# Kernel optimization log

Hardware: AMD Instinct MI355X
Metric: run time of the kernel (lower is better)

Reference implementation:

```python
import jax, jax.numpy as jnp
import numpy as np

GAMMA = 1.0  # offset scaling factor (init kwarg gamma)


def setup_inputs() -> dict:
    key = jax.random.key(0)
    k1, k2, k3 = jax.random.split(key, 3)
    B, C, L, n = 32, 256, 8192, 2048
    inp = jax.random.normal(k1, (B, C, L), dtype=jnp.float32)
    # sampling positions in pixel units, uniform over [0, L-1]
    point = jax.random.uniform(k2, (B, n, 1), dtype=jnp.float32) * (L - 1)
    offset = jax.random.normal(k3, (B, n, 1), dtype=jnp.float32)
    return {"input": inp, "point": point, "offset": offset}


def reference(input, point, offset):
    B, C, L = input.shape
    # (B, n) fractional sampling locations, clamped to valid range
    locs = jnp.clip(point[..., 0] + GAMMA * offset[..., 0], 0.0, L - 1)
    idx0 = jnp.clip(jnp.floor(locs).astype(jnp.int32), 0, L - 1)
    idx1 = jnp.clip(jnp.ceil(locs).astype(jnp.int32), 0, L - 1)
    w1 = locs - idx0.astype(locs.dtype)  # (B, n)
    w0 = 1.0 - w1
    # gather along length axis: (B, C, n)
    g0 = jnp.take_along_axis(input, idx0[:, None, :], axis=2)
    g1 = jnp.take_along_axis(input, idx1[:, None, :], axis=2)
    out = w0[:, None, :] * g0 + w1[:, None, :] * g1  # (B, C, n)
    return jnp.transpose(out, (0, 2, 1))  # (B, n, C)
```

## Files before the change

### kernel.cpp

```cpp
#include <hip/hip_runtime.h>


constexpr int   kB     = 32;
constexpr int   kC     = 256;
constexpr int   kL     = 8192;
constexpr int   kN     = 2048;
constexpr float kGamma = 1.0f;

constexpr int kLt   = 32;
constexpr int kT    = kL / kLt;
constexpr int kCap  = 64;
constexpr int kNXCD = 8;

__global__ __launch_bounds__(256) void fused_sampler_kernel(
    const float* __restrict__ input,
    const float* __restrict__ point,
    const float* __restrict__ offset,
    float* __restrict__ out)
{
    constexpr int kStride = kLt + 1;
    __shared__ float lds[kC * kStride];
    __shared__ int2  mlist[kCap];
    __shared__ int   mcnt;

    constexpr int nwg = kB * kT;
    constexpr int cpx = nwg / kNXCD;
    int wg = blockIdx.x;
    wg = (wg % kNXCD) * cpx + wg / kNXCD;

    const int b   = wg >> 8;
    const int t   = wg & (kT - 1);
    const int tid = threadIdx.x;

    if (tid == 0) mcnt = 0;
    __syncthreads();

    const float* base = input + (size_t)b * kC * kL + t * kLt;
    float4 vals[8];
    #pragma unroll
    for (int k = 0; k < 8; ++k) {
        const int flat4 = k * 256 + tid;
        const int c     = flat4 >> 3;
        const int col4  = flat4 & 7;
        vals[k] = *reinterpret_cast<const float4*>(base + (size_t)c * kL + col4 * 4);
    }
    int gcol = t * kLt + kLt;
    if (gcol > kL - 1) gcol = kL - 1;
    const float halo = input[((size_t)(b * kC + tid)) * kL + gcol];

    {
        const int p0 = tid * 8;
        const float* pp = point  + (size_t)b * kN + p0;
        const float* op = offset + (size_t)b * kN + p0;
        const float4 pA = *reinterpret_cast<const float4*>(pp);
        const float4 pB = *reinterpret_cast<const float4*>(pp + 4);
        const float4 oA = *reinterpret_cast<const float4*>(op);
        const float4 oB = *reinterpret_cast<const float4*>(op + 4);
        float locs[8] = { pA.x + kGamma * oA.x, pA.y + kGamma * oA.y,
                          pA.z + kGamma * oA.z, pA.w + kGamma * oA.w,
                          pB.x + kGamma * oB.x, pB.y + kGamma * oB.y,
                          pB.z + kGamma * oB.z, pB.w + kGamma * oB.w };
        #pragma unroll
        for (int j = 0; j < 8; ++j) {
            float loc = fminf(fmaxf(locs[j], 0.0f), (float)(kL - 1));
            const int idx0 = (int)floorf(loc);
            if ((idx0 >> 5) == t) {
                const int slot = atomicAdd(&mcnt, 1);
                if (slot < kCap)
                    mlist[slot] = make_int2(p0 + j, __float_as_int(loc));
            }
        }
    }

    #pragma unroll
    for (int k = 0; k < 8; ++k) {
        const int flat4 = k * 256 + tid;
        const int c     = flat4 >> 3;
        const int col4  = flat4 & 7;
        float* dst = &lds[c * kStride + col4 * 4];
        dst[0] = vals[k].x; dst[1] = vals[k].y; dst[2] = vals[k].z; dst[3] = vals[k].w;
    }
    lds[tid * kStride + kLt] = halo;
    __syncthreads();

    const int cnt = min(mcnt, kCap);
    for (int e = 0; e < cnt; ++e) {
        const int2 ent  = mlist[e];
        const int   p    = ent.x;
        const float loc  = __int_as_float(ent.y);
        const int   idx0 = (int)floorf(loc);
        const float w1   = loc - (float)idx0;
        const float w0   = 1.0f - w1;
        const int   li   = idx0 - t * kLt;
        const float g0 = lds[tid * kStride + li];
        const float g1 = lds[tid * kStride + li + 1];
        out[((size_t)b * kN + p) * kC + tid] = w0 * g0 + w1 * g1;
    }
}

extern "C" void kernel_launch(void* const* d_in, const int* in_sizes, int n_in,
                              void* d_out, int out_size, void* d_ws, size_t ws_size,
                              hipStream_t stream)
{
    const float* input  = (const float*)d_in[0];
    const float* point  = (const float*)d_in[1];
    const float* offset = (const float*)d_in[2];
    float* out = (float*)d_out;

    fused_sampler_kernel<<<kB * kT, 256, 0, stream>>>(input, point, offset, out);
}
```

Measured before the change: 68.91 us.

## Process eight L-tiles per workgroup with register double-buffered prefetch

Each workgroup now walks eight consecutive 32-column tiles instead of one. While one tile is being sampled out of LDS, the next tile is held in registers and the one after is already being loaded. Point/offset binning is done once per group into per-tile lists, which removes the 8x redundant scan of all 2048 points that one-tile-per-workgroup needed. The grid shrinks to 1024 workgroups and the XCD remapping is dropped. In exchange the kernel uses more registers (occupancy hint of 4), has less parallelism, and caps each tile's list at 48 entries, which risks dropping points when a tile is dense.

```diff
diff --git a/kernel.cpp b/kernel.cpp
--- a/kernel.cpp
+++ b/kernel.cpp
@@ -7,12 +7,12 @@
 constexpr int   kN     = 2048;
 constexpr float kGamma = 1.0f;
 
-constexpr int kLt   = 32;
-constexpr int kT    = kL / kLt;
-constexpr int kCap  = 64;
-constexpr int kNXCD = 8;
+constexpr int kLt     = 32;
+constexpr int kTG     = 8;
+constexpr int kGroups = kL / (kLt * kTG);
+constexpr int kCap    = 48;
 
-__global__ __launch_bounds__(256) void fused_sampler_kernel(
+__global__ __launch_bounds__(256, 4) void fused_sampler_kernel(
     const float* __restrict__ input,
     const float* __restrict__ point,
     const float* __restrict__ offset,
@@ -20,33 +20,38 @@
 {
     constexpr int kStride = kLt + 1;
     __shared__ float lds[kC * kStride];
-    __shared__ int2  mlist[kCap];
-    __shared__ int   mcnt;
+    __shared__ int2  mlist[kTG][kCap];
+    __shared__ int   mcnt[kTG];
 
-    constexpr int nwg = kB * kT;
-    constexpr int cpx = nwg / kNXCD;
-    int wg = blockIdx.x;
-    wg = (wg % kNXCD) * cpx + wg / kNXCD;
+    const int wg  = blockIdx.x;
+    const int b   = wg >> 5;
+    const int tg  = wg & (kGroups - 1);
+    const int tid = threadIdx.x;
+    const int col0 = tg * (kLt * kTG);
 
-    const int b   = wg >> 8;
-    const int t   = wg & (kT - 1);
-    const int tid = threadIdx.x;
-
-    if (tid == 0) mcnt = 0;
+    if (tid < kTG) mcnt[tid] = 0;
     __syncthreads();
 
-    const float* base = input + (size_t)b * kC * kL + t * kLt;
-    float4 vals[8];
+    const float* bbase = input + (size_t)b * kC * kL;
+
+    float4 A[8], B[8];
     #pragma unroll
     for (int k = 0; k < 8; ++k) {
         const int flat4 = k * 256 + tid;
         const int c     = flat4 >> 3;
         const int col4  = flat4 & 7;
-        vals[k] = *reinterpret_cast<const float4*>(base + (size_t)c * kL + col4 * 4);
+        A[k] = *reinterpret_cast<const float4*>(bbase + (size_t)c * kL + col0 + col4 * 4);
     }
-    int gcol = t * kLt + kLt;
+    #pragma unroll
+    for (int k = 0; k < 8; ++k) {
+        const int flat4 = k * 256 + tid;
+        const int c     = flat4 >> 3;
+        const int col4  = flat4 & 7;
+        B[k] = *reinterpret_cast<const float4*>(bbase + (size_t)c * kL + col0 + kLt + col4 * 4);
+    }
+    int gcol = col0 + kLt * kTG;
     if (gcol > kL - 1) gcol = kL - 1;
-    const float halo = input[((size_t)(b * kC + tid)) * kL + gcol];
+    const float h7 = bbase[(size_t)tid * kL + gcol];
 
     {
         const int p0 = tid * 8;
@@ -56,46 +61,81 @@
         const float4 pB = *reinterpret_cast<const float4*>(pp + 4);
         const float4 oA = *reinterpret_cast<const float4*>(op);
         const float4 oB = *reinterpret_cast<const float4*>(op + 4);
-        float locs[8] = { pA.x + kGamma * oA.x, pA.y + kGamma * oA.y,
-                          pA.z + kGamma * oA.z, pA.w + kGamma * oA.w,
-                          pB.x + kGamma * oB.x, pB.y + kGamma * oB.y,
-                          pB.z + kGamma * oB.z, pB.w + kGamma * oB.w };
+        const float locs[8] = { pA.x + kGamma * oA.x, pA.y + kGamma * oA.y,
+                                pA.z + kGamma * oA.z, pA.w + kGamma * oA.w,
+                                pB.x + kGamma * oB.x, pB.y + kGamma * oB.y,
+                                pB.z + kGamma * oB.z, pB.w + kGamma * oB.w };
         #pragma unroll
         for (int j = 0; j < 8; ++j) {
             float loc = fminf(fmaxf(locs[j], 0.0f), (float)(kL - 1));
             const int idx0 = (int)floorf(loc);
-            if ((idx0 >> 5) == t) {
-                const int slot = atomicAdd(&mcnt, 1);
+            const int rng  = (idx0 >> 5) - tg * kTG;
+            if ((unsigned)rng < (unsigned)kTG) {
+                const int slot = atomicAdd(&mcnt[rng], 1);
                 if (slot < kCap)
-                    mlist[slot] = make_int2(p0 + j, __float_as_int(loc));
+                    mlist[rng][slot] = make_int2(p0 + j, __float_as_int(loc));
             }
         }
     }
 
-    #pragma unroll
-    for (int k = 0; k < 8; ++k) {
-        const int flat4 = k * 256 + tid;
-        const int c     = flat4 >> 3;
-        const int col4  = flat4 & 7;
-        float* dst = &lds[c * kStride + col4 * 4];
-        dst[0] = vals[k].x; dst[1] = vals[k].y; dst[2] = vals[k].z; dst[3] = vals[k].w;
-    }
-    lds[tid * kStride + kLt] = halo;
-    __syncthreads();
+    auto tile_phase = [&](const int tt, float4 (&curr)[8], float4 (&next)[8]) {
+        if (tt > 0) __syncthreads();
 
-    const int cnt = min(mcnt, kCap);
-    for (int e = 0; e < cnt; ++e) {
-        const int2 ent  = mlist[e];
-        const int   p    = ent.x;
-        const float loc  = __int_as_float(ent.y);
-        const int   idx0 = (int)floorf(loc);
-        const float w1   = loc - (float)idx0;
-        const float w0   = 1.0f - w1;
-        const int   li   = idx0 - t * kLt;
-        const float g0 = lds[tid * kStride + li];
-        const float g1 = lds[tid * kStride + li + 1];
-        out[((size_t)b * kN + p) * kC + tid] = w0 * g0 + w1 * g1;
-    }
+        #pragma unroll
+        for (int k = 0; k < 8; ++k) {
+            const int flat4 = k * 256 + tid;
+            const int c     = flat4 >> 3;
+            const int col4  = flat4 & 7;
+            float* dst = &lds[c * kStride + col4 * 4];
+            dst[0] = curr[k].x; dst[1] = curr[k].y; dst[2] = curr[k].z; dst[3] = curr[k].w;
+        }
+        if (tt < kTG - 1) {
+            if ((tid & 7) == 0) {
+                #pragma unroll
+                for (int k = 0; k < 8; ++k) {
+                    const int c = (k * 256 + tid) >> 3;
+                    lds[c * kStride + kLt] = next[k].x;
+                }
+            }
+        } else {
+            lds[tid * kStride + kLt] = h7;
+        }
+        __syncthreads();
+
+        if (tt < kTG - 2) {
+            const int colb = col0 + (tt + 2) * kLt;
+            #pragma unroll
+            for (int k = 0; k < 8; ++k) {
+                const int flat4 = k * 256 + tid;
+                const int c     = flat4 >> 3;
+                const int col4  = flat4 & 7;
+                curr[k] = *reinterpret_cast<const float4*>(bbase + (size_t)c * kL + colb + col4 * 4);
+            }
+        }
+
+        const int cnt = min(mcnt[tt], kCap);
+        for (int e = 0; e < cnt; ++e) {
+            const int2 ent  = mlist[tt][e];
+            const int   p    = ent.x;
+            const float loc  = __int_as_float(ent.y);
+            const int   idx0 = (int)floorf(loc);
+            const float w1   = loc - (float)idx0;
+            const float w0   = 1.0f - w1;
+            const int   li   = idx0 - (col0 + tt * kLt);
+            const float g0 = lds[tid * kStride + li];
+            const float g1 = lds[tid * kStride + li + 1];
+            out[((size_t)b * kN + p) * kC + tid] = w0 * g0 + w1 * g1;
+        }
+    };
+
+    tile_phase(0, A, B);
+    tile_phase(1, B, A);
+    tile_phase(2, A, B);
+    tile_phase(3, B, A);
+    tile_phase(4, A, B);
+    tile_phase(5, B, A);
+    tile_phase(6, A, B);
+    tile_phase(7, B, A);
 }
 
 extern "C" void kernel_launch(void* const* d_in, const int* in_sizes, int n_in,
@@ -107,5 +147,5 @@
     const float* offset = (const float*)d_in[2];
     float* out = (float*)d_out;
 
-    fused_sampler_kernel<<<kB * kT, 256, 0, stream>>>(input, point, offset, out);
+    fused_sampler_kernel<<<kB * kGroups, 256, 0, stream>>>(input, point, offset, out);
 }
```

Measured after the change: 69.05 us. No clear change (+0.2%).

## Split tiles by channel group and widen length tiles, parallelize point loop

Applied to the files above, without the earlier changes.

Each workgroup now handles 32 channels over a 128-column length tile instead of all 256 channels over 32 columns. The matched-point loop is spread across eight 32-lane groups, so each group processes different points. This shrinks LDS use to raise occupancy and gives longer contiguous row reads. In exchange, every workgroup still scans all point/offset data, doubling that redundant traffic, and output stores become 128-byte segments.

```diff
diff --git a/kernel.cpp b/kernel.cpp
--- a/kernel.cpp
+++ b/kernel.cpp
@@ -7,46 +7,54 @@
 constexpr int   kN     = 2048;
 constexpr float kGamma = 1.0f;
 
-constexpr int kLt   = 32;
+constexpr int kCh   = 32;
+constexpr int kCG   = kC / kCh;
+constexpr int kLt   = 128;
 constexpr int kT    = kL / kLt;
-constexpr int kCap  = 64;
+constexpr int kCap  = 96;
 constexpr int kNXCD = 8;
 
-__global__ __launch_bounds__(256) void fused_sampler_kernel(
+__global__ __launch_bounds__(256, 8) void fused_sampler_kernel(
     const float* __restrict__ input,
     const float* __restrict__ point,
     const float* __restrict__ offset,
     float* __restrict__ out)
 {
     constexpr int kStride = kLt + 1;
-    __shared__ float lds[kC * kStride];
+    __shared__ float lds[kCh * kStride];
     __shared__ int2  mlist[kCap];
     __shared__ int   mcnt;
 
-    constexpr int nwg = kB * kT;
+    constexpr int nwg = kB * kCG * kT;
     constexpr int cpx = nwg / kNXCD;
     int wg = blockIdx.x;
     wg = (wg % kNXCD) * cpx + wg / kNXCD;
 
-    const int b   = wg >> 8;
-    const int t   = wg & (kT - 1);
-    const int tid = threadIdx.x;
+    const int b    = wg >> 9;
+    const int rem  = wg & 511;
+    const int cg   = rem >> 6;
+    const int t    = rem & (kT - 1);
+    const int tid  = threadIdx.x;
 
     if (tid == 0) mcnt = 0;
     __syncthreads();
 
-    const float* base = input + (size_t)b * kC * kL + t * kLt;
-    float4 vals[8];
+    const float* base = input + (size_t)(b * kC + cg * kCh) * kL + t * kLt;
+
+    float4 v[4];
     #pragma unroll
-    for (int k = 0; k < 8; ++k) {
+    for (int k = 0; k < 4; ++k) {
         const int flat4 = k * 256 + tid;
-        const int c     = flat4 >> 3;
-        const int col4  = flat4 & 7;
-        vals[k] = *reinterpret_cast<const float4*>(base + (size_t)c * kL + col4 * 4);
+        const int row   = flat4 >> 5;
+        const int col4  = flat4 & 31;
+        v[k] = *reinterpret_cast<const float4*>(base + (size_t)row * kL + col4 * 4);
     }
-    int gcol = t * kLt + kLt;
-    if (gcol > kL - 1) gcol = kL - 1;
-    const float halo = input[((size_t)(b * kC + tid)) * kL + gcol];
+    float halo = 0.0f;
+    if (tid < kCh) {
+        int gc = t * kLt + kLt;
+        if (gc > kL - 1) gc = kL - 1;
+        halo = input[(size_t)(b * kC + cg * kCh + tid) * kL + gc];
+    }
 
     {
         const int p0 = tid * 8;
@@ -56,15 +64,16 @@
         const float4 pB = *reinterpret_cast<const float4*>(pp + 4);
         const float4 oA = *reinterpret_cast<const float4*>(op);
         const float4 oB = *reinterpret_cast<const float4*>(op + 4);
-        float locs[8] = { pA.x + kGamma * oA.x, pA.y + kGamma * oA.y,
-                          pA.z + kGamma * oA.z, pA.w + kGamma * oA.w,
-                          pB.x + kGamma * oB.x, pB.y + kGamma * oB.y,
-                          pB.z + kGamma * oB.z, pB.w + kGamma * oB.w };
+        const float locs[8] = { pA.x + kGamma * oA.x, pA.y + kGamma * oA.y,
+                                pA.z + kGamma * oA.z, pA.w + kGamma * oA.w,
+                                pB.x + kGamma * oB.x, pB.y + kGamma * oB.y,
+                                pB.z + kGamma * oB.z, pB.w + kGamma * oB.w };
         #pragma unroll
         for (int j = 0; j < 8; ++j) {
             float loc = fminf(fmaxf(locs[j], 0.0f), (float)(kL - 1));
             const int idx0 = (int)floorf(loc);
-            if ((idx0 >> 5) == t) {
+            const int li   = idx0 - t * kLt;
+            if ((unsigned)li < (unsigned)kLt) {
                 const int slot = atomicAdd(&mcnt, 1);
                 if (slot < kCap)
                     mlist[slot] = make_int2(p0 + j, __float_as_int(loc));
@@ -73,18 +82,20 @@
     }
 
     #pragma unroll
-    for (int k = 0; k < 8; ++k) {
+    for (int k = 0; k < 4; ++k) {
         const int flat4 = k * 256 + tid;
-        const int c     = flat4 >> 3;
-        const int col4  = flat4 & 7;
-        float* dst = &lds[c * kStride + col4 * 4];
-        dst[0] = vals[k].x; dst[1] = vals[k].y; dst[2] = vals[k].z; dst[3] = vals[k].w;
+        const int row   = flat4 >> 5;
+        const int col4  = flat4 & 31;
+        float* dst = &lds[row * kStride + col4 * 4];
+        dst[0] = v[k].x; dst[1] = v[k].y; dst[2] = v[k].z; dst[3] = v[k].w;
     }
-    lds[tid * kStride + kLt] = halo;
+    if (tid < kCh) lds[tid * kStride + kLt] = halo;
     __syncthreads();
 
     const int cnt = min(mcnt, kCap);
-    for (int e = 0; e < cnt; ++e) {
+    const int hw  = tid >> 5;
+    const int c   = tid & 31;
+    for (int e = hw; e < cnt; e += 8) {
         const int2 ent  = mlist[e];
         const int   p    = ent.x;
         const float loc  = __int_as_float(ent.y);
@@ -92,9 +103,9 @@
         const float w1   = loc - (float)idx0;
         const float w0   = 1.0f - w1;
         const int   li   = idx0 - t * kLt;
-        const float g0 = lds[tid * kStride + li];
-        const float g1 = lds[tid * kStride + li + 1];
-        out[((size_t)b * kN + p) * kC + tid] = w0 * g0 + w1 * g1;
+        const float g0 = lds[c * kStride + li];
+        const float g1 = lds[c * kStride + li + 1];
+        out[((size_t)b * kN + p) * kC + cg * kCh + c] = w0 * g0 + w1 * g1;
     }
 }
 
@@ -107,5 +118,5 @@
     const float* offset = (const float*)d_in[2];
     float* out = (float*)d_out;
 
-    fused_sampler_kernel<<<kB * kT, 256, 0, stream>>>(input, point, offset, out);
+    fused_sampler_kernel<<<kB * kCG * kT, 256, 0, stream>>>(input, point, offset, out);
 }
```

New measurement: 66.61 us. 3.3% less time.
